# Kernel optimization log

Hardware: AMD Instinct MI355X
Metric: run time of the kernel (lower is better)

The kernel has to match this reference:

```python
import jax, jax.numpy as jnp
import numpy as np

B, HW, N, C, F, ITERS = 32, 4096, 16, 128, 512, 3
EPS_LN = 1e-5
EPS_ATTN = 1e-5


def _ln(x, g, b):
    m = x.mean(-1, keepdims=True)
    v = ((x - m) ** 2).mean(-1, keepdims=True)
    return (x - m) / jnp.sqrt(v + EPS_LN) * g + b


def _gru(x, h, wih, whh, bih, bhh):
    # torch.nn.GRUCell math
    gi = x @ wih.T + bih
    gh = h @ whh.T + bhh
    i_r, i_z, i_n = jnp.split(gi, 3, axis=-1)
    h_r, h_z, h_n = jnp.split(gh, 3, axis=-1)
    r = jax.nn.sigmoid(i_r + h_r)
    z = jax.nn.sigmoid(i_z + h_z)
    n = jnp.tanh(i_n + r * h_n)
    return (1.0 - z) * n + z * h


def setup_inputs() -> dict:
    key = jax.random.key(0)
    ks = jax.random.split(key, 16)
    s = 0.02
    d = {
        'inp': jax.random.normal(ks[0], (B, HW, C), jnp.float32),
        'query': jax.random.normal(ks[1], (B, N, C), jnp.float32),
        'ln_kv_g': jnp.ones((C,), jnp.float32),
        'ln_kv_b': jnp.zeros((C,), jnp.float32),
        'Wk': jax.random.normal(ks[2], (C, C), jnp.float32) * s,
        'Wv': jax.random.normal(ks[3], (C, C), jnp.float32) * s,
        'ln_q_g': jnp.ones((C,), jnp.float32),
        'ln_q_b': jnp.zeros((C,), jnp.float32),
        'Wq': jax.random.normal(ks[4], (C, C), jnp.float32) * s,
        'gru_wih': jax.random.normal(ks[5], (3 * C, C), jnp.float32) * s,
        'gru_whh': jax.random.normal(ks[6], (3 * C, C), jnp.float32) * s,
        'gru_bih': jnp.zeros((3 * C,), jnp.float32),
        'gru_bhh': jnp.zeros((3 * C,), jnp.float32),
        'ln2_g': jnp.ones((C,), jnp.float32),
        'ln2_b': jnp.zeros((C,), jnp.float32),
        'ffn_w1': jax.random.normal(ks[7], (F, C), jnp.float32) * s,
        'ffn_b1': jnp.zeros((F,), jnp.float32),
        'ffn_w2': jax.random.normal(ks[8], (C, F), jnp.float32) * s,
        'ffn_b2': jnp.zeros((C,), jnp.float32),
    }
    return d


def reference(inp, query, ln_kv_g, ln_kv_b, Wk, Wv, ln_q_g, ln_q_b, Wq,
              gru_wih, gru_whh, gru_bih, gru_bhh, ln2_g, ln2_b,
              ffn_w1, ffn_b1, ffn_w2, ffn_b2):
    b, n, c = query.shape
    kv = _ln(inp, ln_kv_g, ln_kv_b)
    k = kv @ Wk.T  # (b, hw, c)
    v = kv @ Wv.T  # (b, hw, c)
    scale = c ** -0.5
    q = query
    a0 = None
    for _ in range(ITERS):
        x = q
        qn = _ln(q, ln_q_g, ln_q_b) @ Wq.T
        logit = jnp.einsum('bqc,bkc->bqk', qn * scale, k)  # (b, n, hw)
        a0 = jax.nn.softmax(logit, axis=1)  # inverted: softmax over slots
        a = a0 / (a0.sum(2, keepdims=True) + EPS_ATTN)  # renorm over keys
        u = jnp.einsum('bqk,bkc->bqc', a, v)
        y = _gru(u.reshape(b * n, c), x.reshape(b * n, c),
                 gru_wih, gru_whh, gru_bih, gru_bhh).reshape(b, n, c)
        z = _ln(y, ln2_g, ln2_b)
        ffn = jax.nn.relu(z @ ffn_w1.T + ffn_b1) @ ffn_w2.T + ffn_b2
        q = y + ffn
    return (q, a0)
```

## Files before the change

kernel.cpp:

```cpp
#include <hip/hip_runtime.h>
#include <math.h>

#define B_ 32
#define HW_ 4096
#define N_ 16
#define C_ 128
#define F_ 512
#define ITERS_ 3
#define EPS_LN 1e-5f
#define EPS_ATTN 1e-5f

typedef __attribute__((ext_vector_type(8))) short short8;
typedef __attribute__((ext_vector_type(4))) float f32x4;

static __device__ __forceinline__ unsigned short f2b(float f) {
    union { float f; unsigned u; } v; v.f = f;
    unsigned r = v.u + 0x7fffu + ((v.u >> 16) & 1u);
    return (unsigned short)(r >> 16);
}
static __device__ __forceinline__ float blo(unsigned u) {
    union { unsigned u; float f; } v; v.u = u << 16; return v.f;
}
static __device__ __forceinline__ float bhi(unsigned u) {
    union { unsigned u; float f; } v; v.u = u & 0xffff0000u; return v.f;
}

__global__ __launch_bounds__(256) void k_prep(
    const float* __restrict__ Wk, const float* __restrict__ Wv,
    const float* __restrict__ wih, const float* __restrict__ whh,
    const float* __restrict__ w1, const float* __restrict__ w2,
    unsigned short* __restrict__ Wk_bf, unsigned short* __restrict__ Wv_bf,
    unsigned short* __restrict__ wih_bf, unsigned short* __restrict__ whh_bf,
    unsigned short* __restrict__ w1_bf, unsigned short* __restrict__ w2_bf,
    const float* __restrict__ query, const float* __restrict__ lnqg,
    const float* __restrict__ lnqb, const float* __restrict__ Wq,
    unsigned short* __restrict__ qn_g)
{
    __shared__ __align__(16) float xq[16 * 128];
    int tid = threadIdx.x;
    if (blockIdx.x < 256) {
        int t = blockIdx.x * 256 + tid;
        const float* src; unsigned short* dst; int off;
        if (t < 4096)       { src = Wk;  dst = Wk_bf;  off = t; }
        else if (t < 8192)  { src = Wv;  dst = Wv_bf;  off = t - 4096; }
        else if (t < 20480) { src = wih; dst = wih_bf; off = t - 8192; }
        else if (t < 32768) { src = whh; dst = whh_bf; off = t - 20480; }
        else if (t < 49152) { src = w1;  dst = w1_bf;  off = t - 32768; }
        else                { src = w2;  dst = w2_bf;  off = t - 49152; }
        float4 a = ((const float4*)src)[off];
        uint2 p;
        p.x = (unsigned)f2b(a.x) | ((unsigned)f2b(a.y) << 16);
        p.y = (unsigned)f2b(a.z) | ((unsigned)f2b(a.w) << 16);
        *(uint2*)(dst + off * 4) = p;
        return;
    }
    int b = blockIdx.x - 256;
    int n = tid >> 4, part = tid & 15;
    int row = b * 16 + n;
    const float4* x4 = (const float4*)(query + row * 128 + part * 8);
    float4 x0 = x4[0], x1 = x4[1];
    float s = x0.x + x0.y + x0.z + x0.w + x1.x + x1.y + x1.z + x1.w;
    float ss = x0.x * x0.x + x0.y * x0.y + x0.z * x0.z + x0.w * x0.w +
               x1.x * x1.x + x1.y * x1.y + x1.z * x1.z + x1.w * x1.w;
    s += __shfl_xor(s, 1); s += __shfl_xor(s, 2); s += __shfl_xor(s, 4); s += __shfl_xor(s, 8);
    ss += __shfl_xor(ss, 1); ss += __shfl_xor(ss, 2); ss += __shfl_xor(ss, 4); ss += __shfl_xor(ss, 8);
    float mean = s * (1.f / 128.f);
    float var = ss * (1.f / 128.f) - mean * mean;
    float rstd = rsqrtf(var + EPS_LN);
    const float4* g4 = (const float4*)(lnqg + part * 8);
    const float4* b4 = (const float4*)(lnqb + part * 8);
    float4 g0 = g4[0], g1 = g4[1], bb0 = b4[0], bb1 = b4[1];
    float4 o0, o1;
    o0.x = (x0.x - mean) * rstd * g0.x + bb0.x;
    o0.y = (x0.y - mean) * rstd * g0.y + bb0.y;
    o0.z = (x0.z - mean) * rstd * g0.z + bb0.z;
    o0.w = (x0.w - mean) * rstd * g0.w + bb0.w;
    o1.x = (x1.x - mean) * rstd * g1.x + bb1.x;
    o1.y = (x1.y - mean) * rstd * g1.y + bb1.y;
    o1.z = (x1.z - mean) * rstd * g1.z + bb1.z;
    o1.w = (x1.w - mean) * rstd * g1.w + bb1.w;
    float4* xrow = (float4*)&xq[n * 128];
    xrow[part * 2] = o0;
    xrow[part * 2 + 1] = o1;
    __syncthreads();
    float o[8] = {0.f, 0.f, 0.f, 0.f, 0.f, 0.f, 0.f, 0.f};
    const float4* xv4 = (const float4*)&xq[n * 128];
#pragma unroll 4
    for (int j = 0; j < 32; j++) {
        float4 xv = xv4[j];
#pragma unroll
        for (int i = 0; i < 8; i++) {
            float4 w = ((const float4*)(Wq + (part * 8 + i) * 128))[j];
            o[i] += w.x * xv.x + w.y * xv.y + w.z * xv.z + w.w * xv.w;
        }
    }
    const float scale = 0.08838834764831845f;
#pragma unroll
    for (int i = 0; i < 8; i++)
        qn_g[row * 128 + part * 8 + i] = f2b(o[i] * scale);
}

__global__ __launch_bounds__(256) void k_kvproj(
    const float* __restrict__ inp, const float* __restrict__ lng,
    const float* __restrict__ lnb, const unsigned short* __restrict__ Wk_bf,
    const unsigned short* __restrict__ Wv_bf, unsigned short* __restrict__ Kbf,
    unsigned short* __restrict__ Vt)
{
    __shared__ __align__(16) unsigned short W_lds[128 * 128];
    __shared__ __align__(16) unsigned short T_lds[8960];
    const int tid = threadIdx.x;
    const int wave = tid >> 6, lane = tid & 63;
    const int l15 = lane & 15, q4 = lane >> 4;
    const int kof = q4 * 8;
    const int tile0 = blockIdx.x * 64;
    const int b = tile0 >> 12;
    const int hwbase = tile0 & (HW_ - 1);

    const int srow = tid >> 1, shalf = tid & 1;
    const int sswz = srow & 7;

    float x[4][8];
    {
        const float* rowp = inp + (tile0 + (wave << 4) + l15) * C_;
        float s = 0.f, ss = 0.f;
#pragma unroll
        for (int ks = 0; ks < 4; ks++) {
#pragma unroll
            for (int h = 0; h < 2; h++) {
                float4 v = *(const float4*)(rowp + ks * 32 + kof + h * 4);
                x[ks][h * 4 + 0] = v.x; x[ks][h * 4 + 1] = v.y;
                x[ks][h * 4 + 2] = v.z; x[ks][h * 4 + 3] = v.w;
                s += v.x + v.y + v.z + v.w;
                ss += v.x * v.x + v.y * v.y + v.z * v.z + v.w * v.w;
            }
        }
        s += __shfl_xor(s, 16);  s += __shfl_xor(s, 32);
        ss += __shfl_xor(ss, 16); ss += __shfl_xor(ss, 32);
        float mean = s * (1.f / 128.f);
        float var = ss * (1.f / 128.f) - mean * mean;
        float rstd = rsqrtf(var + EPS_LN);
#pragma unroll
        for (int ks = 0; ks < 4; ks++) {
#pragma unroll
            for (int h = 0; h < 2; h++) {
                float4 g = *(const float4*)(lng + ks * 32 + kof + h * 4);
                float4 bb = *(const float4*)(lnb + ks * 32 + kof + h * 4);
                x[ks][h * 4 + 0] = (x[ks][h * 4 + 0] - mean) * rstd * g.x + bb.x;
                x[ks][h * 4 + 1] = (x[ks][h * 4 + 1] - mean) * rstd * g.y + bb.y;
                x[ks][h * 4 + 2] = (x[ks][h * 4 + 2] - mean) * rstd * g.z + bb.z;
                x[ks][h * 4 + 3] = (x[ks][h * 4 + 3] - mean) * rstd * g.w + bb.w;
            }
        }
    }
    short8 af[4];
#pragma unroll
    for (int ks = 0; ks < 4; ks++) {
        union { short8 s8; unsigned u[4]; } p;
#pragma unroll
        for (int j = 0; j < 4; j++)
            p.u[j] = (unsigned)f2b(x[ks][2 * j]) | ((unsigned)f2b(x[ks][2 * j + 1]) << 16);
        af[ks] = p.s8;
    }

    {
        const uint4* gW = (const uint4*)Wk_bf;
#pragma unroll
        for (int j = 0; j < 8; j++) {
            int c = shalf * 8 + j;
            uint4 w = gW[srow * 16 + c];
            *(uint4*)&W_lds[srow * 128 + (c ^ sswz) * 8] = w;
        }
    }
    __syncthreads();

    f32x4 acc[8];
#pragma unroll
    for (int nt = 0; nt < 8; nt++) {
        acc[nt] = (f32x4){0.f, 0.f, 0.f, 0.f};
#pragma unroll
        for (int ks = 0; ks < 4; ks++) {
            short8 bf = *(const short8*)&W_lds[(nt * 16 + l15) * 128 + ((ks * 4 + q4) ^ (l15 & 7)) * 8];
            acc[nt] = __builtin_amdgcn_mfma_f32_16x16x32_bf16(af[ks], bf, acc[nt], 0, 0, 0);
        }
    }
#pragma unroll
    for (int nt = 0; nt < 8; nt++) {
        int c = nt * 16 + l15;
#pragma unroll
        for (int i = 0; i < 4; i++)
            T_lds[((wave << 4) + (q4 << 2) + i) * 132 + c] = f2b(acc[nt][i]);
    }
    __syncthreads();
    {
        int row = tid >> 2, part = tid & 3;
        uint4* dst = (uint4*)&Kbf[(b * HW_ + hwbase + row) * C_ + part * 32];
#pragma unroll
        for (int j = 0; j < 4; j++)
            dst[j] = *(const uint4*)&T_lds[row * 132 + part * 32 + j * 8];
    }
    {
        const uint4* gW = (const uint4*)Wv_bf;
#pragma unroll
        for (int j = 0; j < 8; j++) {
            int c = shalf * 8 + j;
            uint4 w = gW[srow * 16 + c];
            *(uint4*)&W_lds[srow * 128 + (c ^ sswz) * 8] = w;
        }
    }
    __syncthreads();
#pragma unroll
    for (int nt = 0; nt < 8; nt++) {
        acc[nt] = (f32x4){0.f, 0.f, 0.f, 0.f};
#pragma unroll
        for (int ks = 0; ks < 4; ks++) {
            short8 bf = *(const short8*)&W_lds[(nt * 16 + l15) * 128 + ((ks * 4 + q4) ^ (l15 & 7)) * 8];
            acc[nt] = __builtin_amdgcn_mfma_f32_16x16x32_bf16(af[ks], bf, acc[nt], 0, 0, 0);
        }
    }
    __syncthreads();
#pragma unroll
    for (int nt = 0; nt < 8; nt++) {
        int c = nt * 16 + l15;
#pragma unroll
        for (int i = 0; i < 4; i++)
            T_lds[c * 70 + (wave << 4) + (q4 << 2) + i] = f2b(acc[nt][i]);
    }
    __syncthreads();
    {
        int c = tid >> 1, half = tid & 1;
        uint4* dst = (uint4*)&Vt[(b * C_ + c) * HW_ + hwbase + half * 32];
#pragma unroll
        for (int j = 0; j < 4; j++)
            dst[j] = *(const uint4*)&T_lds[c * 70 + half * 32 + j * 8];
    }
}

__global__ __launch_bounds__(256) void k_attn(
    const unsigned short* __restrict__ qn_g, const unsigned short* __restrict__ Kbf,
    const unsigned short* __restrict__ Vt, float* __restrict__ Upart,
    float* __restrict__ rspart, float* __restrict__ a0_out, int last)
{
    __shared__ __align__(16) float Ul[4][2048];
    __shared__ float rsw[4][16];
    const int b = blockIdx.y, chunk = blockIdx.x;
    const int tid = threadIdx.x;
    const int wave = tid >> 6, lane = tid & 63;
    const int l15 = lane & 15, q4 = lane >> 4;
    const int kof = q4 * 8;
    const int hwb = chunk * 128 + wave * 32;

    unsigned short* Pw = (unsigned short*)&Ul[wave][0];

    short8 aq[4];
#pragma unroll
    for (int ks = 0; ks < 4; ks++)
        aq[ks] = *(const short8*)&qn_g[(b * 16 + l15) * 128 + ks * 32 + kof];
    short8 av[8];
#pragma unroll
    for (int ct = 0; ct < 8; ct++)
        av[ct] = *(const short8*)&Vt[(b * C_ + ct * 16 + l15) * HW_ + hwb + kof];

    float rs[4] = {0.f, 0.f, 0.f, 0.f};
#pragma unroll
    for (int s = 0; s < 2; s++) {
        int hwt = hwb + s * 16;
        f32x4 sa = {0.f, 0.f, 0.f, 0.f};
#pragma unroll
        for (int ks = 0; ks < 4; ks++) {
            short8 bk = *(const short8*)&Kbf[(b * HW_ + hwt + l15) * C_ + ks * 32 + kof];
            sa = __builtin_amdgcn_mfma_f32_16x16x32_bf16(aq[ks], bk, sa, 0, 0, 0);
        }
        float mx = fmaxf(fmaxf(sa[0], sa[1]), fmaxf(sa[2], sa[3]));
        mx = fmaxf(mx, __shfl_xor(mx, 16));
        mx = fmaxf(mx, __shfl_xor(mx, 32));
        float e[4]; float ssum = 0.f;
#pragma unroll
        for (int i = 0; i < 4; i++) { e[i] = __expf(sa[i] - mx); ssum += e[i]; }
        ssum += __shfl_xor(ssum, 16);
        ssum += __shfl_xor(ssum, 32);
        float inv = 1.f / ssum;
#pragma unroll
        for (int i = 0; i < 4; i++) {
            float a0v = e[i] * inv;
            rs[i] += a0v;
            if (last) a0_out[(b * 16 + q4 * 4 + i) * HW_ + hwt + l15] = a0v;
            Pw[(q4 * 4 + i) * 40 + s * 16 + l15] = f2b(a0v);
        }
    }
#pragma unroll
    for (int i = 0; i < 4; i++) {
        rs[i] += __shfl_xor(rs[i], 1);
        rs[i] += __shfl_xor(rs[i], 2);
        rs[i] += __shfl_xor(rs[i], 4);
        rs[i] += __shfl_xor(rs[i], 8);
    }
    if (l15 == 0) {
#pragma unroll
        for (int i = 0; i < 4; i++) rsw[wave][q4 * 4 + i] = rs[i];
    }
    short8 bp = *(const short8*)&Pw[l15 * 40 + kof];
#pragma unroll
    for (int ct = 0; ct < 8; ct++) {
        f32x4 ua = __builtin_amdgcn_mfma_f32_16x16x32_bf16(av[ct], bp, (f32x4){0.f, 0.f, 0.f, 0.f}, 0, 0, 0);
        int c = ct * 16 + q4 * 4;
#pragma unroll
        for (int i = 0; i < 4; i++)
            Ul[wave][(c + i) * 16 + l15] = ua[i];
    }
    __syncthreads();
    {
        float* up = Upart + (b * 32 + chunk) * 2048;
#pragma unroll
        for (int k = 0; k < 8; k++) {
            int idx = tid + k * 256;
            up[idx] = Ul[0][idx] + Ul[1][idx] + Ul[2][idx] + Ul[3][idx];
        }
        if (tid < 16)
            rspart[(b * 32 + chunk) * 16 + tid] =
                rsw[0][tid] + rsw[1][tid] + rsw[2][tid] + rsw[3][tid];
    }
}

__global__ __launch_bounds__(256) void k_tail(
    const float* __restrict__ Upart, const float* __restrict__ rspart,
    const float* __restrict__ hsrc, float* __restrict__ q_buf,
    const unsigned short* __restrict__ wih_bf, const unsigned short* __restrict__ whh_bf,
    const float* __restrict__ bih, const float* __restrict__ bhh,
    const float* __restrict__ ln2g, const float* __restrict__ ln2b,
    const unsigned short* __restrict__ w1_bf, const float* __restrict__ b1,
    const unsigned short* __restrict__ w2_bf, const float* __restrict__ b2,
    const float* __restrict__ lnqg, const float* __restrict__ lnqb,
    const float* __restrict__ Wq, unsigned short* __restrict__ qn_g,
    float* __restrict__ out_q, int last)
{
    __shared__ __align__(16) float u_l[128];
    __shared__ __align__(16) float h_l[128];
    __shared__ __align__(16) float g_l[768];
    __shared__ __align__(16) float z_l[128];
    __shared__ __align__(16) float y_l[128];
    __shared__ __align__(16) float h1_l[512];
    __shared__ __align__(16) float red[256];
    __shared__ float stats[2];
    __shared__ float srs;
    const int tid = threadIdx.x;
    const int row = blockIdx.x;
    const int b = row >> 4, q = row & 15;
    const int lane = tid & 63;

    {
        int c = tid & 127, h = tid >> 7;
        float part = 0.f;
#pragma unroll
        for (int ch = 0; ch < 16; ch++)
            part += Upart[(b * 32 + h * 16 + ch) * 2048 + c * 16 + q];
        red[tid] = part;
        if (tid < 128) h_l[tid] = hsrc[row * 128 + tid];
        if (tid < 64) {
            float v = (lane < 32) ? rspart[(b * 32 + lane) * 16 + q] : 0.f;
#pragma unroll
            for (int off = 1; off < 64; off <<= 1) v += __shfl_xor(v, off);
            if (tid == 0) srs = v;
        }
    }
    __syncthreads();
    if (tid < 128)
        u_l[tid] = (red[tid] + red[tid + 128]) / (srs + EPS_ATTN);
    __syncthreads();
#pragma unroll
    for (int o3 = 0; o3 < 3; o3++) {
        int o = tid + o3 * 256;
        const unsigned short* wrow;
        const float* src;
        float bias;
        if (o < 384) { wrow = wih_bf + o * 128; src = u_l; bias = bih[o]; }
        else         { wrow = whh_bf + (o - 384) * 128; src = h_l; bias = bhh[o - 384]; }
        const uint4* w4 = (const uint4*)wrow;
        const float4* s4 = (const float4*)src;
        float acc = 0.f;
#pragma unroll 8
        for (int j = 0; j < 16; j++) {
            uint4 w = w4[j];
            float4 aA = s4[2 * j], aB = s4[2 * j + 1];
            acc += blo(w.x) * aA.x + bhi(w.x) * aA.y + blo(w.y) * aA.z + bhi(w.y) * aA.w
                 + blo(w.z) * aB.x + bhi(w.z) * aB.y + blo(w.w) * aB.z + bhi(w.w) * aB.w;
        }
        g_l[o] = acc + bias;
    }
    __syncthreads();
    if (tid < 128) {
        int c = tid;
        float ir = g_l[c], iz = g_l[128 + c], in_ = g_l[256 + c];
        float hr = g_l[384 + c], hz = g_l[512 + c], hn = g_l[640 + c];
        float rr = 1.f / (1.f + expf(-(ir + hr)));
        float zz = 1.f / (1.f + expf(-(iz + hz)));
        float nn = tanhf(in_ + rr * hn);
        y_l[c] = (1.f - zz) * nn + zz * h_l[c];
    }
    __syncthreads();
    if (tid < 64) {
        float v0 = y_l[lane], v1 = y_l[lane + 64];
        float s = v0 + v1, ss = v0 * v0 + v1 * v1;
#pragma unroll
        for (int off = 1; off < 64; off <<= 1) {
            s += __shfl_xor(s, off);
            ss += __shfl_xor(ss, off);
        }
        if (tid == 0) {
            float mean = s * (1.f / 128.f);
            float var = ss * (1.f / 128.f) - mean * mean;
            stats[0] = mean;
            stats[1] = rsqrtf(var + EPS_LN);
        }
    }
    __syncthreads();
    if (tid < 128)
        z_l[tid] = (y_l[tid] - stats[0]) * stats[1] * ln2g[tid] + ln2b[tid];
    __syncthreads();
#pragma unroll
    for (int f2i = 0; f2i < 2; f2i++) {
        int f = tid + f2i * 256;
        const uint4* w4 = (const uint4*)(w1_bf + f * 128);
        const float4* s4 = (const float4*)z_l;
        float acc = 0.f;
#pragma unroll 8
        for (int j = 0; j < 16; j++) {
            uint4 w = w4[j];
            float4 aA = s4[2 * j], aB = s4[2 * j + 1];
            acc += blo(w.x) * aA.x + bhi(w.x) * aA.y + blo(w.y) * aA.z + bhi(w.y) * aA.w
                 + blo(w.z) * aB.x + bhi(w.z) * aB.y + blo(w.w) * aB.z + bhi(w.w) * aB.w;
        }
        h1_l[f] = fmaxf(acc + b1[f], 0.f);
    }
    __syncthreads();
    {
        int c = tid & 127, h = tid >> 7;
        const uint4* w4 = (const uint4*)(w2_bf + c * 512 + h * 256);
        const float4* hh = (const float4*)&h1_l[h * 256];
        float acc = 0.f;
#pragma unroll 8
        for (int j = 0; j < 32; j++) {
            uint4 w = w4[j];
            float4 hA = hh[2 * j], hB = hh[2 * j + 1];
            acc += blo(w.x) * hA.x + bhi(w.x) * hA.y + blo(w.y) * hA.z + bhi(w.y) * hA.w
                 + blo(w.z) * hB.x + bhi(w.z) * hB.y + blo(w.w) * hB.z + bhi(w.w) * hB.w;
        }
        red[tid] = acc;
    }
    __syncthreads();
    float q_new = 0.f;
    if (tid < 128) {
        q_new = y_l[tid] + red[tid] + red[tid + 128] + b2[tid];
        q_buf[row * 128 + tid] = q_new;
        if (last) out_q[row * 128 + tid] = q_new;
    }
    if (!last) {
        __syncthreads();
        if (tid < 128) y_l[tid] = q_new;
        __syncthreads();
        if (tid < 64) {
            float v0 = y_l[lane], v1 = y_l[lane + 64];
            float s = v0 + v1, ss = v0 * v0 + v1 * v1;
#pragma unroll
            for (int off = 1; off < 64; off <<= 1) {
                s += __shfl_xor(s, off);
                ss += __shfl_xor(ss, off);
            }
            if (tid == 0) {
                float mean = s * (1.f / 128.f);
                float var = ss * (1.f / 128.f) - mean * mean;
                stats[0] = mean;
                stats[1] = rsqrtf(var + EPS_LN);
            }
        }
        __syncthreads();
        if (tid < 128)
            z_l[tid] = (y_l[tid] - stats[0]) * stats[1] * lnqg[tid] + lnqb[tid];
        __syncthreads();
        {
            int c = tid & 127, h = tid >> 7;
            const float4* w4 = (const float4*)(Wq + c * 128 + h * 64);
            const float4* zz = (const float4*)&z_l[h * 64];
            float acc = 0.f;
#pragma unroll 8
            for (int j = 0; j < 16; j++) {
                float4 w = w4[j], v = zz[j];
                acc += w.x * v.x + w.y * v.y + w.z * v.z + w.w * v.w;
            }
            red[tid] = acc;
        }
        __syncthreads();
        if (tid < 128)
            qn_g[row * 128 + tid] = f2b((red[tid] + red[tid + 128]) * 0.08838834764831845f);
    }
}

extern "C" void kernel_launch(void* const* d_in, const int* in_sizes, int n_in,
                              void* d_out, int out_size, void* d_ws, size_t ws_size,
                              hipStream_t stream) {
    const float* inp     = (const float*)d_in[0];
    const float* query   = (const float*)d_in[1];
    const float* ln_kv_g = (const float*)d_in[2];
    const float* ln_kv_b = (const float*)d_in[3];
    const float* Wk      = (const float*)d_in[4];
    const float* Wv      = (const float*)d_in[5];
    const float* ln_q_g  = (const float*)d_in[6];
    const float* ln_q_b  = (const float*)d_in[7];
    const float* Wq      = (const float*)d_in[8];
    const float* gru_wih = (const float*)d_in[9];
    const float* gru_whh = (const float*)d_in[10];
    const float* gru_bih = (const float*)d_in[11];
    const float* gru_bhh = (const float*)d_in[12];
    const float* ln2_g   = (const float*)d_in[13];
    const float* ln2_b   = (const float*)d_in[14];
    const float* ffn_w1  = (const float*)d_in[15];
    const float* ffn_b1  = (const float*)d_in[16];
    const float* ffn_w2  = (const float*)d_in[17];
    const float* ffn_b2  = (const float*)d_in[18];

    char* ws = (char*)d_ws;
    unsigned short* Kbf    = (unsigned short*)ws;
    unsigned short* Vt     = (unsigned short*)(ws + 33554432);
    float* q_buf           = (float*)(ws + 67108864);
    float* Upart           = (float*)(ws + 67371008);
    float* rspart          = (float*)(ws + 75759616);
    unsigned short* qn_g   = (unsigned short*)(ws + 75825152);
    unsigned short* Wk_bf  = (unsigned short*)(ws + 75956224);
    unsigned short* Wv_bf  = (unsigned short*)(ws + 75988992);
    unsigned short* wih_bf = (unsigned short*)(ws + 76021760);
    unsigned short* whh_bf = (unsigned short*)(ws + 76120064);
    unsigned short* w1_bf  = (unsigned short*)(ws + 76218368);
    unsigned short* w2_bf  = (unsigned short*)(ws + 76349440);

    float* out_q  = (float*)d_out;
    float* out_a0 = out_q + B_ * N_ * C_;

    k_prep<<<dim3(288), dim3(256), 0, stream>>>(
        Wk, Wv, gru_wih, gru_whh, ffn_w1, ffn_w2,
        Wk_bf, Wv_bf, wih_bf, whh_bf, w1_bf, w2_bf,
        query, ln_q_g, ln_q_b, Wq, qn_g);
    k_kvproj<<<dim3((B_ * HW_) / 64), dim3(256), 0, stream>>>(
        inp, ln_kv_g, ln_kv_b, Wk_bf, Wv_bf, Kbf, Vt);

    for (int it = 0; it < ITERS_; it++) {
        int last = (it == ITERS_ - 1) ? 1 : 0;
        const float* hsrc = (it == 0) ? query : q_buf;
        k_attn<<<dim3(32, B_), dim3(256), 0, stream>>>(
            qn_g, Kbf, Vt, Upart, rspart, out_a0, last);
        k_tail<<<dim3(B_ * N_), dim3(256), 0, stream>>>(
            Upart, rspart, hsrc, q_buf, wih_bf, whh_bf, gru_bih, gru_bhh,
            ln2_g, ln2_b, w1_bf, ffn_b1, w2_bf, ffn_b2,
            ln_q_g, ln_q_b, Wq, qn_g, out_q, last);
    }
}
```

Measured before the change: 350.4 us.

## Split K/V projection across blocks and reduce attention partials with LDS atomics

The KV projection kernel is restructured so each block loads only one weight matrix (Wk or Wv) into LDS once and processes four 64-row tiles. Outputs are written straight from MFMA registers, using a swapped operand order for K so no LDS transpose staging is needed. Each input tile now gets its layernorm and bf16 conversion twice, once in a K block and once in a V block, doubling reads of the input. In the attention kernel, the four per-wave U partial buffers are replaced by a single padded LDS buffer accumulated with atomicAdd, shrinking LDS footprint and changing the Upart layout, which the tail kernel reads accordingly.

```diff
diff --git a/kernel.cpp b/kernel.cpp
--- a/kernel.cpp
+++ b/kernel.cpp
@@ -107,131 +107,103 @@
     unsigned short* __restrict__ Vt)
 {
     __shared__ __align__(16) unsigned short W_lds[128 * 128];
-    __shared__ __align__(16) unsigned short T_lds[8960];
     const int tid = threadIdx.x;
     const int wave = tid >> 6, lane = tid & 63;
     const int l15 = lane & 15, q4 = lane >> 4;
     const int kof = q4 * 8;
-    const int tile0 = blockIdx.x * 64;
-    const int b = tile0 >> 12;
-    const int hwbase = tile0 & (HW_ - 1);
-
-    const int srow = tid >> 1, shalf = tid & 1;
-    const int sswz = srow & 7;
-
-    float x[4][8];
+    const int isK = (blockIdx.x < 512);
+    const int blkL = blockIdx.x & 511;
+
     {
-        const float* rowp = inp + (tile0 + (wave << 4) + l15) * C_;
-        float s = 0.f, ss = 0.f;
-#pragma unroll
-        for (int ks = 0; ks < 4; ks++) {
-#pragma unroll
-            for (int h = 0; h < 2; h++) {
-                float4 v = *(const float4*)(rowp + ks * 32 + kof + h * 4);
-                x[ks][h * 4 + 0] = v.x; x[ks][h * 4 + 1] = v.y;
-                x[ks][h * 4 + 2] = v.z; x[ks][h * 4 + 3] = v.w;
-                s += v.x + v.y + v.z + v.w;
-                ss += v.x * v.x + v.y * v.y + v.z * v.z + v.w * v.w;
-            }
-        }
-        s += __shfl_xor(s, 16);  s += __shfl_xor(s, 32);
-        ss += __shfl_xor(ss, 16); ss += __shfl_xor(ss, 32);
-        float mean = s * (1.f / 128.f);
-        float var = ss * (1.f / 128.f) - mean * mean;
-        float rstd = rsqrtf(var + EPS_LN);
-#pragma unroll
-        for (int ks = 0; ks < 4; ks++) {
-#pragma unroll
-            for (int h = 0; h < 2; h++) {
-                float4 g = *(const float4*)(lng + ks * 32 + kof + h * 4);
-                float4 bb = *(const float4*)(lnb + ks * 32 + kof + h * 4);
-                x[ks][h * 4 + 0] = (x[ks][h * 4 + 0] - mean) * rstd * g.x + bb.x;
-                x[ks][h * 4 + 1] = (x[ks][h * 4 + 1] - mean) * rstd * g.y + bb.y;
-                x[ks][h * 4 + 2] = (x[ks][h * 4 + 2] - mean) * rstd * g.z + bb.z;
-                x[ks][h * 4 + 3] = (x[ks][h * 4 + 3] - mean) * rstd * g.w + bb.w;
-            }
-        }
-    }
-    short8 af[4];
-#pragma unroll
-    for (int ks = 0; ks < 4; ks++) {
-        union { short8 s8; unsigned u[4]; } p;
-#pragma unroll
-        for (int j = 0; j < 4; j++)
-            p.u[j] = (unsigned)f2b(x[ks][2 * j]) | ((unsigned)f2b(x[ks][2 * j + 1]) << 16);
-        af[ks] = p.s8;
-    }
-
-    {
-        const uint4* gW = (const uint4*)Wk_bf;
+        const unsigned short* Wsrc = isK ? Wk_bf : Wv_bf;
+        int srow = tid >> 1, shalf = tid & 1, sswz = srow & 7;
+        const uint4* gW = (const uint4*)Wsrc;
 #pragma unroll
         for (int j = 0; j < 8; j++) {
             int c = shalf * 8 + j;
-            uint4 w = gW[srow * 16 + c];
-            *(uint4*)&W_lds[srow * 128 + (c ^ sswz) * 8] = w;
-        }
-    }
-    __syncthreads();
-
-    f32x4 acc[8];
-#pragma unroll
-    for (int nt = 0; nt < 8; nt++) {
-        acc[nt] = (f32x4){0.f, 0.f, 0.f, 0.f};
+            *(uint4*)&W_lds[srow * 128 + (c ^ sswz) * 8] = gW[srow * 16 + c];
+        }
+    }
+    __syncthreads();
+
+#pragma unroll 1
+    for (int t = 0; t < 4; t++) {
+        const int tile0 = (blkL * 4 + t) * 64;
+        const int b = tile0 >> 12;
+        const int hwbase = tile0 & (HW_ - 1);
+
+        float x[4][8];
+        {
+            const float* rowp = inp + (tile0 + (wave << 4) + l15) * C_;
+            float s = 0.f, ss = 0.f;
+#pragma unroll
+            for (int ks = 0; ks < 4; ks++) {
+#pragma unroll
+                for (int h = 0; h < 2; h++) {
+                    float4 v = *(const float4*)(rowp + ks * 32 + kof + h * 4);
+                    x[ks][h * 4 + 0] = v.x; x[ks][h * 4 + 1] = v.y;
+                    x[ks][h * 4 + 2] = v.z; x[ks][h * 4 + 3] = v.w;
+                    s += v.x + v.y + v.z + v.w;
+                    ss += v.x * v.x + v.y * v.y + v.z * v.z + v.w * v.w;
+                }
+            }
+            s += __shfl_xor(s, 16);  s += __shfl_xor(s, 32);
+            ss += __shfl_xor(ss, 16); ss += __shfl_xor(ss, 32);
+            float mean = s * (1.f / 128.f);
+            float var = ss * (1.f / 128.f) - mean * mean;
+            float rstd = rsqrtf(var + EPS_LN);
+#pragma unroll
+            for (int ks = 0; ks < 4; ks++) {
+#pragma unroll
+                for (int h = 0; h < 2; h++) {
+                    float4 g = *(const float4*)(lng + ks * 32 + kof + h * 4);
+                    float4 bb = *(const float4*)(lnb + ks * 32 + kof + h * 4);
+                    x[ks][h * 4 + 0] = (x[ks][h * 4 + 0] - mean) * rstd * g.x + bb.x;
+                    x[ks][h * 4 + 1] = (x[ks][h * 4 + 1] - mean) * rstd * g.y + bb.y;
+                    x[ks][h * 4 + 2] = (x[ks][h * 4 + 2] - mean) * rstd * g.z + bb.z;
+                    x[ks][h * 4 + 3] = (x[ks][h * 4 + 3] - mean) * rstd * g.w + bb.w;
+                }
+            }
+        }
+        short8 af[4];
 #pragma unroll
         for (int ks = 0; ks < 4; ks++) {
-            short8 bf = *(const short8*)&W_lds[(nt * 16 + l15) * 128 + ((ks * 4 + q4) ^ (l15 & 7)) * 8];
-            acc[nt] = __builtin_amdgcn_mfma_f32_16x16x32_bf16(af[ks], bf, acc[nt], 0, 0, 0);
-        }
-    }
-#pragma unroll
-    for (int nt = 0; nt < 8; nt++) {
-        int c = nt * 16 + l15;
-#pragma unroll
-        for (int i = 0; i < 4; i++)
-            T_lds[((wave << 4) + (q4 << 2) + i) * 132 + c] = f2b(acc[nt][i]);
-    }
-    __syncthreads();
-    {
-        int row = tid >> 2, part = tid & 3;
-        uint4* dst = (uint4*)&Kbf[(b * HW_ + hwbase + row) * C_ + part * 32];
-#pragma unroll
-        for (int j = 0; j < 4; j++)
-            dst[j] = *(const uint4*)&T_lds[row * 132 + part * 32 + j * 8];
-    }
-    {
-        const uint4* gW = (const uint4*)Wv_bf;
-#pragma unroll
-        for (int j = 0; j < 8; j++) {
-            int c = shalf * 8 + j;
-            uint4 w = gW[srow * 16 + c];
-            *(uint4*)&W_lds[srow * 128 + (c ^ sswz) * 8] = w;
-        }
-    }
-    __syncthreads();
-#pragma unroll
-    for (int nt = 0; nt < 8; nt++) {
-        acc[nt] = (f32x4){0.f, 0.f, 0.f, 0.f};
-#pragma unroll
-        for (int ks = 0; ks < 4; ks++) {
-            short8 bf = *(const short8*)&W_lds[(nt * 16 + l15) * 128 + ((ks * 4 + q4) ^ (l15 & 7)) * 8];
-            acc[nt] = __builtin_amdgcn_mfma_f32_16x16x32_bf16(af[ks], bf, acc[nt], 0, 0, 0);
-        }
-    }
-    __syncthreads();
-#pragma unroll
-    for (int nt = 0; nt < 8; nt++) {
-        int c = nt * 16 + l15;
-#pragma unroll
-        for (int i = 0; i < 4; i++)
-            T_lds[c * 70 + (wave << 4) + (q4 << 2) + i] = f2b(acc[nt][i]);
-    }
-    __syncthreads();
-    {
-        int c = tid >> 1, half = tid & 1;
-        uint4* dst = (uint4*)&Vt[(b * C_ + c) * HW_ + hwbase + half * 32];
-#pragma unroll
-        for (int j = 0; j < 4; j++)
-            dst[j] = *(const uint4*)&T_lds[c * 70 + half * 32 + j * 8];
+            union { short8 s8; unsigned u[4]; } p;
+#pragma unroll
+            for (int j = 0; j < 4; j++)
+                p.u[j] = (unsigned)f2b(x[ks][2 * j]) | ((unsigned)f2b(x[ks][2 * j + 1]) << 16);
+            af[ks] = p.s8;
+        }
+
+        if (isK) {
+#pragma unroll
+            for (int ct = 0; ct < 8; ct++) {
+                f32x4 acc = {0.f, 0.f, 0.f, 0.f};
+#pragma unroll
+                for (int ks = 0; ks < 4; ks++) {
+                    short8 wf = *(const short8*)&W_lds[(ct * 16 + l15) * 128 + ((ks * 4 + q4) ^ (l15 & 7)) * 8];
+                    acc = __builtin_amdgcn_mfma_f32_16x16x32_bf16(wf, af[ks], acc, 0, 0, 0);
+                }
+                union { uint2 u2; unsigned short sh[4]; } pk;
+#pragma unroll
+                for (int i = 0; i < 4; i++) pk.sh[i] = f2b(acc[i]);
+                *(uint2*)&Kbf[(b * HW_ + hwbase + (wave << 4) + l15) * C_ + ct * 16 + (q4 << 2)] = pk.u2;
+            }
+        } else {
+#pragma unroll
+            for (int nt = 0; nt < 8; nt++) {
+                f32x4 acc = {0.f, 0.f, 0.f, 0.f};
+#pragma unroll
+                for (int ks = 0; ks < 4; ks++) {
+                    short8 wf = *(const short8*)&W_lds[(nt * 16 + l15) * 128 + ((ks * 4 + q4) ^ (l15 & 7)) * 8];
+                    acc = __builtin_amdgcn_mfma_f32_16x16x32_bf16(af[ks], wf, acc, 0, 0, 0);
+                }
+                union { uint2 u2; unsigned short sh[4]; } pv;
+#pragma unroll
+                for (int i = 0; i < 4; i++) pv.sh[i] = f2b(acc[i]);
+                *(uint2*)&Vt[(b * C_ + nt * 16 + l15) * HW_ + hwbase + (wave << 4) + (q4 << 2)] = pv.u2;
+            }
+        }
     }
 }
 
@@ -240,7 +212,8 @@
     const unsigned short* __restrict__ Vt, float* __restrict__ Upart,
     float* __restrict__ rspart, float* __restrict__ a0_out, int last)
 {
-    __shared__ __align__(16) float Ul[4][2048];
+    __shared__ float Ul[16 * 137];
+    __shared__ __align__(16) unsigned short Pb[4][16 * 40];
     __shared__ float rsw[4][16];
     const int b = blockIdx.y, chunk = blockIdx.x;
     const int tid = threadIdx.x;
@@ -249,7 +222,7 @@
     const int kof = q4 * 8;
     const int hwb = chunk * 128 + wave * 32;
 
-    unsigned short* Pw = (unsigned short*)&Ul[wave][0];
+    for (int i = tid; i < 16 * 137; i += 256) Ul[i] = 0.f;
 
     short8 aq[4];
 #pragma unroll
@@ -259,7 +232,9 @@
 #pragma unroll
     for (int ct = 0; ct < 8; ct++)
         av[ct] = *(const short8*)&Vt[(b * C_ + ct * 16 + l15) * HW_ + hwb + kof];
-
+    __syncthreads();
+
+    unsigned short* Pw = &Pb[wave][0];
     float rs[4] = {0.f, 0.f, 0.f, 0.f};
 #pragma unroll
     for (int s = 0; s < 2; s++) {
@@ -302,10 +277,10 @@
 #pragma unroll
     for (int ct = 0; ct < 8; ct++) {
         f32x4 ua = __builtin_amdgcn_mfma_f32_16x16x32_bf16(av[ct], bp, (f32x4){0.f, 0.f, 0.f, 0.f}, 0, 0, 0);
-        int c = ct * 16 + q4 * 4;
+        int c = ct * 16 + (q4 << 2);
 #pragma unroll
         for (int i = 0; i < 4; i++)
-            Ul[wave][(c + i) * 16 + l15] = ua[i];
+            atomicAdd(&Ul[l15 * 137 + c + i], ua[i]);
     }
     __syncthreads();
     {
@@ -313,7 +288,7 @@
 #pragma unroll
         for (int k = 0; k < 8; k++) {
             int idx = tid + k * 256;
-            up[idx] = Ul[0][idx] + Ul[1][idx] + Ul[2][idx] + Ul[3][idx];
+            up[idx] = Ul[(idx >> 7) * 137 + (idx & 127)];
         }
         if (tid < 16)
             rspart[(b * 32 + chunk) * 16 + tid] =
@@ -352,7 +327,7 @@
         float part = 0.f;
 #pragma unroll
         for (int ch = 0; ch < 16; ch++)
-            part += Upart[(b * 32 + h * 16 + ch) * 2048 + c * 16 + q];
+            part += Upart[(b * 32 + h * 16 + ch) * 2048 + q * 128 + c];
         red[tid] = part;
         if (tid < 128) h_l[tid] = hsrc[row * 128 + tid];
         if (tid < 64) {
@@ -538,7 +513,7 @@
         Wk, Wv, gru_wih, gru_whh, ffn_w1, ffn_w2,
         Wk_bf, Wv_bf, wih_bf, whh_bf, w1_bf, w2_bf,
         query, ln_q_g, ln_q_b, Wq, qn_g);
-    k_kvproj<<<dim3((B_ * HW_) / 64), dim3(256), 0, stream>>>(
+    k_kvproj<<<dim3(1024), dim3(256), 0, stream>>>(
         inp, ln_kv_g, ln_kv_b, Wk_bf, Wv_bf, Kbf, Vt);
 
     for (int it = 0; it < ITERS_; it++) {
```

After: 455.8 us. 1.3x slower.

## Halve attn block to 2 waves with 64 keys each and slot-major Upart

Applied to the files above, without the earlier changes.

k_attn now launches 128 threads (2 waves) per block. Each wave handles 64 keys instead of 32 and accumulates two K=32 MFMAs into one U tile, which halves the per-block LDS cross-wave reduction. Partial U is stored slot-major with a padded stride so each lane writes an f32x4 vector, and k_tail's read is updated to match, giving coalesced reads over c. The cost is fewer waves per block and higher register pressure from the larger V fragment array, which may reduce latency hiding.

```diff
diff --git a/kernel.cpp b/kernel.cpp
--- a/kernel.cpp
+++ b/kernel.cpp
@@ -235,34 +235,37 @@
     }
 }
 
-__global__ __launch_bounds__(256) void k_attn(
+__global__ __launch_bounds__(128) void k_attn(
     const unsigned short* __restrict__ qn_g, const unsigned short* __restrict__ Kbf,
     const unsigned short* __restrict__ Vt, float* __restrict__ Upart,
     float* __restrict__ rspart, float* __restrict__ a0_out, int last)
 {
-    __shared__ __align__(16) float Ul[4][2048];
-    __shared__ float rsw[4][16];
+    __shared__ __align__(16) float Ul[2][16 * 132];
+    __shared__ __align__(16) unsigned short Pb[2][16 * 72];
+    __shared__ float rsw[2][16];
     const int b = blockIdx.y, chunk = blockIdx.x;
     const int tid = threadIdx.x;
     const int wave = tid >> 6, lane = tid & 63;
     const int l15 = lane & 15, q4 = lane >> 4;
     const int kof = q4 * 8;
-    const int hwb = chunk * 128 + wave * 32;
-
-    unsigned short* Pw = (unsigned short*)&Ul[wave][0];
+    const int hwb = chunk * 128 + wave * 64;
 
     short8 aq[4];
 #pragma unroll
     for (int ks = 0; ks < 4; ks++)
         aq[ks] = *(const short8*)&qn_g[(b * 16 + l15) * 128 + ks * 32 + kof];
-    short8 av[8];
-#pragma unroll
-    for (int ct = 0; ct < 8; ct++)
-        av[ct] = *(const short8*)&Vt[(b * C_ + ct * 16 + l15) * HW_ + hwb + kof];
-
+    short8 av[8][2];
+#pragma unroll
+    for (int ct = 0; ct < 8; ct++) {
+#pragma unroll
+        for (int k2 = 0; k2 < 2; k2++)
+            av[ct][k2] = *(const short8*)&Vt[(b * C_ + ct * 16 + l15) * HW_ + hwb + k2 * 32 + kof];
+    }
+
+    unsigned short* Pw = &Pb[wave][0];
     float rs[4] = {0.f, 0.f, 0.f, 0.f};
 #pragma unroll
-    for (int s = 0; s < 2; s++) {
+    for (int s = 0; s < 4; s++) {
         int hwt = hwb + s * 16;
         f32x4 sa = {0.f, 0.f, 0.f, 0.f};
 #pragma unroll
@@ -284,7 +287,7 @@
             float a0v = e[i] * inv;
             rs[i] += a0v;
             if (last) a0_out[(b * 16 + q4 * 4 + i) * HW_ + hwt + l15] = a0v;
-            Pw[(q4 * 4 + i) * 40 + s * 16 + l15] = f2b(a0v);
+            Pw[(q4 * 4 + i) * 72 + s * 16 + l15] = f2b(a0v);
         }
     }
 #pragma unroll
@@ -298,26 +301,25 @@
 #pragma unroll
         for (int i = 0; i < 4; i++) rsw[wave][q4 * 4 + i] = rs[i];
     }
-    short8 bp = *(const short8*)&Pw[l15 * 40 + kof];
+    short8 bp0 = *(const short8*)&Pw[l15 * 72 + kof];
+    short8 bp1 = *(const short8*)&Pw[l15 * 72 + 32 + kof];
 #pragma unroll
     for (int ct = 0; ct < 8; ct++) {
-        f32x4 ua = __builtin_amdgcn_mfma_f32_16x16x32_bf16(av[ct], bp, (f32x4){0.f, 0.f, 0.f, 0.f}, 0, 0, 0);
-        int c = ct * 16 + q4 * 4;
-#pragma unroll
-        for (int i = 0; i < 4; i++)
-            Ul[wave][(c + i) * 16 + l15] = ua[i];
+        f32x4 ua = __builtin_amdgcn_mfma_f32_16x16x32_bf16(av[ct][0], bp0, (f32x4){0.f, 0.f, 0.f, 0.f}, 0, 0, 0);
+        ua = __builtin_amdgcn_mfma_f32_16x16x32_bf16(av[ct][1], bp1, ua, 0, 0, 0);
+        *(f32x4*)&Ul[wave][l15 * 132 + ct * 16 + (q4 << 2)] = ua;
     }
     __syncthreads();
     {
         float* up = Upart + (b * 32 + chunk) * 2048;
 #pragma unroll
-        for (int k = 0; k < 8; k++) {
-            int idx = tid + k * 256;
-            up[idx] = Ul[0][idx] + Ul[1][idx] + Ul[2][idx] + Ul[3][idx];
+        for (int k = 0; k < 16; k++) {
+            int idx = tid + k * 128;
+            int q = idx >> 7, c = idx & 127;
+            up[idx] = Ul[0][q * 132 + c] + Ul[1][q * 132 + c];
         }
         if (tid < 16)
-            rspart[(b * 32 + chunk) * 16 + tid] =
-                rsw[0][tid] + rsw[1][tid] + rsw[2][tid] + rsw[3][tid];
+            rspart[(b * 32 + chunk) * 16 + tid] = rsw[0][tid] + rsw[1][tid];
     }
 }
 
@@ -352,7 +354,7 @@
         float part = 0.f;
 #pragma unroll
         for (int ch = 0; ch < 16; ch++)
-            part += Upart[(b * 32 + h * 16 + ch) * 2048 + c * 16 + q];
+            part += Upart[(b * 32 + h * 16 + ch) * 2048 + q * 128 + c];
         red[tid] = part;
         if (tid < 128) h_l[tid] = hsrc[row * 128 + tid];
         if (tid < 64) {
@@ -544,7 +546,7 @@
     for (int it = 0; it < ITERS_; it++) {
         int last = (it == ITERS_ - 1) ? 1 : 0;
         const float* hsrc = (it == 0) ? query : q_buf;
-        k_attn<<<dim3(32, B_), dim3(256), 0, stream>>>(
+        k_attn<<<dim3(32, B_), dim3(128), 0, stream>>>(
             qn_g, Kbf, Vt, Upart, rspart, out_a0, last);
         k_tail<<<dim3(B_ * N_), dim3(256), 0, stream>>>(
             Upart, rspart, hsrc, q_buf, wih_bf, whh_bf, gru_bih, gru_bhh,
```

Measured after the change: 332.4 us. 1.05x faster.
